# Kernel tuning notes

Hardware: AMD Instinct MI355X
Metric: run time of the kernel (lower is better)

## Reference

```python
import jax, jax.numpy as jnp
import numpy as np

EPS = 1e-5

def dwconv(x, w):
    # x: (B,C,T), w: (C,1,3) depthwise, stride 1, pad 1
    return jax.lax.conv_general_dilated(
        x, w, window_strides=(1,), padding=[(1, 1)],
        dimension_numbers=('NCH', 'OIH', 'NCH'),
        feature_group_count=x.shape[1])

def chan_ln(x, w, b):
    # LayerNorm over channel dim (axis=1) of (B,C,T)
    mu = jnp.mean(x, axis=1, keepdims=True)
    r = x - mu
    sigma = jnp.mean(r * r, axis=1, keepdims=True)
    return (r / jnp.sqrt(sigma + EPS)) * w + b

def conv1x1(x, w, b):
    # x: (B,C,T), w: (O,C), b: (O,)
    return jnp.einsum('oc,bct->bot', w, x) + b[None, :, None]

def setup_inputs() -> dict:
    B, C, T, H = 4, 1024, 1024, 16
    key0 = jax.random.key(0)
    ks = jax.random.split(key0, 16)
    s = 0.02
    inp = {
        'query': jax.random.normal(ks[0], (B, C, T), jnp.float32),
        'key': jax.random.normal(ks[1], (B, C, T), jnp.float32),
        'value': jax.random.normal(ks[2], (B, C, T), jnp.float32),
        'query_mask': jnp.ones((B, 1, T), jnp.bool_),
        'kv_mask': jnp.ones((B, 1, T), jnp.bool_),
        # depthwise conv weights (C,1,3), no bias
        'qconv_w': jax.random.normal(ks[3], (C, 1, 3), jnp.float32) * s,
        'kconv_w': jax.random.normal(ks[4], (C, 1, 3), jnp.float32) * s,
        'vconv_w': jax.random.normal(ks[5], (C, 1, 3), jnp.float32) * s,
        # channel LayerNorm affine params (1,C,1)
        'qn_w': jnp.ones((1, C, 1), jnp.float32), 'qn_b': jnp.zeros((1, C, 1), jnp.float32),
        'kn_w': jnp.ones((1, C, 1), jnp.float32), 'kn_b': jnp.zeros((1, C, 1), jnp.float32),
        'vn_w': jnp.ones((1, C, 1), jnp.float32), 'vn_b': jnp.zeros((1, C, 1), jnp.float32),
        # 1x1 conv (= per-timestep linear) weights (C,C) + bias (C,)
        'wq': jax.random.normal(ks[6], (C, C), jnp.float32) * s, 'bq': jnp.zeros((C,), jnp.float32),
        'wk': jax.random.normal(ks[7], (C, C), jnp.float32) * s, 'bk': jnp.zeros((C,), jnp.float32),
        'wv': jax.random.normal(ks[8], (C, C), jnp.float32) * s, 'bv': jnp.zeros((C,), jnp.float32),
        'wp': jax.random.normal(ks[9], (C, C), jnp.float32) * s, 'bp': jnp.zeros((C,), jnp.float32),
    }
    return inp

def reference(query, key, value, query_mask, kv_mask,
              qconv_w, kconv_w, vconv_w,
              qn_w, qn_b, kn_w, kn_b, vn_w, vn_b,
              wq, bq, wk, bk, wv, bv, wp, bp):
    B, C, T = query.shape
    H = 16
    ch = C // H
    scale = 1.0 / jnp.sqrt(jnp.asarray(ch, query.dtype))
    qm = query_mask.astype(query.dtype)   # (B,1,T), stride 1 -> qx_mask == query_mask
    kvm = kv_mask.astype(query.dtype)

    q = chan_ln(dwconv(query, qconv_w) * qm, qn_w, qn_b)
    k = chan_ln(dwconv(key, kconv_w) * kvm, kn_w, kn_b)
    v = chan_ln(dwconv(value, vconv_w) * kvm, vn_w, vn_b)

    q = conv1x1(q, wq, bq)
    k = conv1x1(k, wk, bk)
    v = conv1x1(v, wv, bv)

    # (B,C,T) -> (B,H,T,ch)
    q = q.reshape(B, H, ch, T).transpose(0, 1, 3, 2)
    k = k.reshape(B, H, ch, T).transpose(0, 1, 3, 2)
    v = v.reshape(B, H, ch, T).transpose(0, 1, 3, 2)

    att = jax.nn.softmax(jnp.einsum('bhsc,bhtc->bhst', q, k) * scale, axis=-1)
    # post-softmax mask applied to V (not to scores) — faithful to the original
    vm = v * kvm[:, :, :, None]           # (B,1,T)->(B,1,T,1) broadcast over heads/ch
    out = jnp.einsum('bhst,bhtc->bhsc', att, vm)

    out = out.transpose(0, 1, 3, 2).reshape(B, C, T)
    out = conv1x1(out, wp, bp) * qm
    return out, query_mask
```

## Files before the change

kernel.cpp:

```cpp
#include <hip/hip_runtime.h>
#include <math.h>

#define B_ 4
#define C_ 1024
#define T_ 1024
#define H_ 16
#define CH_ 64
#define BCT (B_ * C_ * T_)

typedef __attribute__((ext_vector_type(8))) short s16x8;
typedef __attribute__((ext_vector_type(4))) float f32x4;
typedef __attribute__((ext_vector_type(2))) float f32x2;
typedef unsigned short u16;
typedef unsigned char u8;

#define MFMA16(a, b, c) __builtin_amdgcn_mfma_f32_16x16x32_bf16((a), (b), (c), 0, 0, 0)
#define MFMA8(a, b, c)  __builtin_amdgcn_mfma_f32_16x16x32_fp8_fp8((a), (b), (c), 0, 0, 0)

extern "C" __device__ float __ocml_native_exp2_f32(float);

__device__ __forceinline__ u16 f2bf(float f) {
    union { float f; unsigned u; } v; v.f = f;
    unsigned r = (v.u + 0x7fffu + ((v.u >> 16) & 1u)) >> 16;
    return (u16)r;
}
__device__ __forceinline__ float bf2f(u16 h) {
    union { unsigned u; float f; } v; v.u = (unsigned)h << 16; return v.f;
}

__device__ __forceinline__ unsigned pk4_fp8(float a, float b, float c, float d) {
    int v = 0;
    v = __builtin_amdgcn_cvt_pk_fp8_f32(a, b, v, false);
    v = __builtin_amdgcn_cvt_pk_fp8_f32(c, d, v, true);
    return (unsigned)v;
}

typedef __attribute__((address_space(3))) unsigned int lds_u32;
typedef __attribute__((address_space(1))) const unsigned int glb_u32;
__device__ __forceinline__ void glds16(const void* g, const void* l_wave_uniform) {
    __builtin_amdgcn_global_load_lds(
        (glb_u32*)(unsigned long long)g,
        (lds_u32*)(unsigned long long)l_wave_uniform, 16, 0, 0);
}

#define WAIT_BARRIER(N)                                   \
    asm volatile("s_waitcnt vmcnt(" #N ")" ::: "memory"); \
    __builtin_amdgcn_s_barrier();                         \
    __builtin_amdgcn_sched_barrier(0)

__global__ __launch_bounds__(512) void prep_kernel(
    const float* __restrict__ xq, const float* __restrict__ xk, const float* __restrict__ xv,
    const float* __restrict__ wq3, const float* __restrict__ wk3, const float* __restrict__ wv3,
    const int* __restrict__ qm, const int* __restrict__ kvm,
    const float* __restrict__ qnw, const float* __restrict__ qnb,
    const float* __restrict__ knw, const float* __restrict__ knb,
    const float* __restrict__ vnw, const float* __restrict__ vnb,
    u8* __restrict__ oq, u8* __restrict__ ok, u8* __restrict__ ov,
    const float* __restrict__ w0, const float* __restrict__ w1,
    const float* __restrict__ w2, const float* __restrict__ w3,
    u8* __restrict__ o0, u8* __restrict__ o1, u8* __restrict__ o2, u16* __restrict__ o3,
    float* __restrict__ tail_out, int ntail)
{
    __shared__ __align__(16) u8 tile8[32 * 1040];
    __shared__ float w3L[3072];
    __shared__ float red1[16][33], red2[16][33];
    __shared__ float musL[32], rssL[32];

    const int bid = blockIdx.x;
    if (bid >= 384) {
        if (bid >= 2432) {
            int i = (bid - 2432) * 512 + threadIdx.x;
            if (i < ntail) tail_out[i] = (qm[i] != 0) ? 1.f : 0.f;
            return;
        }
        const int b2 = bid - 384;
        const int mat = b2 >> 9;
        const int i = ((b2 & 511) * 512 + threadIdx.x) * 4;
        if (mat == 3) {
            float4 v = *(const float4*)&w3[i];
            uint2 p;
            p.x = (unsigned)f2bf(v.x) | ((unsigned)f2bf(v.y) << 16);
            p.y = (unsigned)f2bf(v.z) | ((unsigned)f2bf(v.w) << 16);
            *(uint2*)&o3[i] = p;
        } else {
            const float* __restrict__ w = (mat == 0) ? w0 : (mat == 1) ? w1 : w2;
            u8* __restrict__ o = (mat == 0) ? o0 : (mat == 1) ? o1 : o2;
            float4 v = *(const float4*)&w[i];
            *(unsigned*)&o[i] = pk4_fp8(64.f * v.x, 64.f * v.y, 64.f * v.z, 64.f * v.w);
        }
        return;
    }

    const int z = bid >> 5;
    const int tensor = z >> 2, b = z & 3;
    const float* __restrict__ x   = (tensor == 0) ? xq  : (tensor == 1) ? xk  : xv;
    const float* __restrict__ w3c = (tensor == 0) ? wq3 : (tensor == 1) ? wk3 : wv3;
    const int* __restrict__ msk   = (tensor == 0) ? qm  : kvm;
    const float* __restrict__ wln = (tensor == 0) ? qnw : (tensor == 1) ? knw : vnw;
    const float* __restrict__ bln = (tensor == 0) ? qnb : (tensor == 1) ? knb : vnb;
    u8* __restrict__ xt = (tensor == 0) ? oq : (tensor == 1) ? ok : ov;

    const int t0 = (bid & 31) * 32;

    #pragma unroll
    for (int i = 0; i < 6; ++i) w3L[i * 512 + threadIdx.x] = w3c[i * 512 + threadIdx.x];
    __syncthreads();

    const int tl = threadIdx.x & 31, cs = threadIdx.x >> 5;
    const int t = t0 + tl;
    const float mk = (msk[b * T_ + t] != 0) ? 1.f : 0.f;

    float s1 = 0.f, s2 = 0.f;
    #pragma unroll 4
    for (int i = 0; i < 32; ++i) {
        const int c = 2 * (cs + 16 * i);
        const float* xr0 = x + ((size_t)(b * C_ + c)) * T_ + t;
        const float* xr1 = xr0 + T_;
        const f32x2 wA = *(const f32x2*)&w3L[3 * c];
        const f32x2 wB = *(const f32x2*)&w3L[3 * c + 2];
        const f32x2 wC = *(const f32x2*)&w3L[3 * c + 4];
        float xc0 = xr0[0];
        float xm0 = (t > 0)      ? xr0[-1] : 0.f;
        float xp0 = (t < T_ - 1) ? xr0[1]  : 0.f;
        float v0 = (wA[0] * xm0 + wA[1] * xc0 + wB[0] * xp0) * mk;
        float xc1 = xr1[0];
        float xm1 = (t > 0)      ? xr1[-1] : 0.f;
        float xp1 = (t < T_ - 1) ? xr1[1]  : 0.f;
        float v1 = (wB[1] * xm1 + wC[0] * xc1 + wC[1] * xp1) * mk;
        s1 += v0 + v1;
        s2 += v0 * v0 + v1 * v1;
        int p2 = __builtin_amdgcn_cvt_pk_fp8_f32(16.f * v0, 16.f * v1, 0, false);
        *(u16*)&tile8[tl * 1040 + c] = (u16)p2;
    }
    red1[cs][tl] = s1;
    red2[cs][tl] = s2;
    __syncthreads();
    if (threadIdx.x < 32) {
        float a = 0.f, q2 = 0.f;
        #pragma unroll
        for (int i = 0; i < 16; ++i) { a += red1[i][threadIdx.x]; q2 += red2[i][threadIdx.x]; }
        float m_  = a  * (1.f / C_);
        float var = q2 * (1.f / C_) - m_ * m_;
        musL[threadIdx.x] = m_;
        rssL[threadIdx.x] = rsqrtf(var + 1e-5f);
    }
    __syncthreads();

    #pragma unroll
    for (int it = 0; it < 8; ++it) {
        const int idx = it * 512 + threadIdx.x;
        const int tt = idx >> 7, c0 = (idx & 127) * 8;
        const uint2 pv8 = *(const uint2*)&tile8[tt * 1040 + c0];
        const f32x2 f01 = __builtin_amdgcn_cvt_pk_f32_fp8((int)pv8.x, false);
        const f32x2 f23 = __builtin_amdgcn_cvt_pk_f32_fp8((int)pv8.x, true);
        const f32x2 f45 = __builtin_amdgcn_cvt_pk_f32_fp8((int)pv8.y, false);
        const f32x2 f67 = __builtin_amdgcn_cvt_pk_f32_fp8((int)pv8.y, true);
        const float m_ = musL[tt], rv = rssL[tt];
        const float4 wv0 = *(const float4*)&wln[c0];
        const float4 wv1 = *(const float4*)&wln[c0 + 4];
        const float4 bv0 = *(const float4*)&bln[c0];
        const float4 bv1 = *(const float4*)&bln[c0 + 4];
        const float inv16 = 0.0625f;
        float fv0 = (f01[0] * inv16 - m_) * rv * wv0.x + bv0.x;
        float fv1 = (f01[1] * inv16 - m_) * rv * wv0.y + bv0.y;
        float fv2 = (f23[0] * inv16 - m_) * rv * wv0.z + bv0.z;
        float fv3 = (f23[1] * inv16 - m_) * rv * wv0.w + bv0.w;
        float fv4 = (f45[0] * inv16 - m_) * rv * wv1.x + bv1.x;
        float fv5 = (f45[1] * inv16 - m_) * rv * wv1.y + bv1.y;
        float fv6 = (f67[0] * inv16 - m_) * rv * wv1.z + bv1.z;
        float fv7 = (f67[1] * inv16 - m_) * rv * wv1.w + bv1.w;
        uint2 o;
        o.x = pk4_fp8(fv0, fv1, fv2, fv3);
        o.y = pk4_fp8(fv4, fv5, fv6, fv7);
        *(uint2*)&xt[((size_t)(b * T_ + t0 + tt)) * C_ + c0] = o;
    }
}

__device__ __forceinline__ void stage_slab8(
    const u8* __restrict__ gA, const u8* __restrict__ gB,
    u8* lA, u8* lB, int k0, int wave, int lane)
{
    const int rl = lane >> 1, h = lane & 1;
    const int row = wave * 32 + rl;
    const int hs = (h ^ ((row >> 2) & 1)) * 16;
    glds16(gA + (size_t)row * C_ + k0 + hs, lA + wave * 1024);
    glds16(gB + (size_t)row * C_ + k0 + hs, lB + wave * 1024);
}

__global__ __launch_bounds__(256) void gemm_qkv_kernel(
    const u8* __restrict__ Xq, const u8* __restrict__ Xk, const u8* __restrict__ Xv,
    const u8* __restrict__ Wq, const u8* __restrict__ Wk, const u8* __restrict__ Wv,
    const float* __restrict__ bq, const float* __restrict__ bk, const float* __restrict__ bv,
    u16* __restrict__ Qt, u16* __restrict__ Kt, u16* __restrict__ Vb, const int* __restrict__ kvm)
{
    const int p = blockIdx.x;
    const int lb = (p & 7) * 96 + (p >> 3);
    const int z = lb >> 6, yy = (lb >> 3) & 7, xx = lb & 7;
    const int tensor = z >> 2, b = z & 3;
    const size_t off = (size_t)b * (1024 * 1024);
    const float qscale = 0.125f * 1.44269504088896340736f;
    const u8* A = (tensor == 0) ? Xq + off : (tensor == 1) ? Xk + off : Wv;
    const u8* B = (tensor == 0) ? Wq       : (tensor == 1) ? Wk       : Xv + off;
    u16*     D = (tensor == 0) ? Qt + off : (tensor == 1) ? Kt + off : Vb + off;
    const float* bias = (tensor == 0) ? bq : (tensor == 1) ? bk : bv;
    const int* mask = (tensor == 2) ? kvm + (size_t)b * T_ : nullptr;
    const float scale = (tensor == 0) ? qscale : 1.f;
    const int bias_on_n = (tensor != 2);
    const int m0 = yy * 128, n0 = xx * 128;

    __shared__ __align__(16) u8 As[3][128 * 32];
    __shared__ __align__(16) u8 Bs[3][128 * 32];
    const int tid = threadIdx.x, lane = tid & 63, wave = tid >> 6;
    const int r = lane & 15, g = lane >> 4;
    const int wm = (wave >> 1) * 64, wn = (wave & 1) * 64;
    const u8* Ab = A + (size_t)m0 * C_;
    const u8* Bb = B + (size_t)n0 * C_;

    f32x4 acc[4][4];
    #pragma unroll
    for (int i = 0; i < 4; ++i)
        #pragma unroll
        for (int j = 0; j < 4; ++j) acc[i][j] = f32x4{0.f, 0.f, 0.f, 0.f};

    stage_slab8(Ab, Bb, As[0], Bs[0], 0, wave, lane);
    stage_slab8(Ab, Bb, As[1], Bs[1], 32, wave, lane);
    WAIT_BARRIER(2);

    const int rsw = ((r >> 2) & 1) << 1;
    const int NK = C_ / 32;
    int cur = 0;
    for (int kk = 0; kk < NK; ++kk) {
        int pre = cur + 2; if (pre >= 3) pre -= 3;
        if (kk + 2 < NK)
            stage_slab8(Ab, Bb, As[pre], Bs[pre], (kk + 2) * 32, wave, lane);
        long af[4], bf[4];
        #pragma unroll
        for (int mi = 0; mi < 4; ++mi)
            af[mi] = *(const long*)&As[cur][(wm + 16 * mi + r) * 32 + ((g ^ rsw) * 8)];
        #pragma unroll
        for (int ni = 0; ni < 4; ++ni)
            bf[ni] = *(const long*)&Bs[cur][(wn + 16 * ni + r) * 32 + ((g ^ rsw) * 8)];
        #pragma unroll
        for (int mi = 0; mi < 4; ++mi)
            #pragma unroll
            for (int ni = 0; ni < 4; ++ni)
                acc[mi][ni] = MFMA8(af[mi], bf[ni], acc[mi][ni]);
        if (kk + 1 < NK) {
            if (kk + 2 < NK) { WAIT_BARRIER(2); }
            else             { WAIT_BARRIER(0); }
        }
        cur = (cur == 2) ? 0 : cur + 1;
    }

    #pragma unroll
    for (int mi = 0; mi < 4; ++mi) {
        #pragma unroll
        for (int ni = 0; ni < 4; ++ni) {
            const int n = n0 + wn + 16 * ni + r;
            float mk = 1.f;
            if (mask) mk = (mask[n] != 0) ? 1.f : 0.f;
            #pragma unroll
            for (int i = 0; i < 4; ++i) {
                const int m = m0 + wm + 16 * mi + 4 * g + i;
                float v = acc[mi][ni][i] * 0.015625f + (bias_on_n ? bias[n] : bias[m]);
                v *= scale * mk;
                D[(size_t)m * 1024 + n] = f2bf(v);
            }
        }
    }
}

__device__ __forceinline__ void stage_slab(
    const u16* __restrict__ gA, const u16* __restrict__ gB,
    u16* lA, u16* lB, int k0, int wave, int lane)
{
    const int rw = lane >> 2, ch = lane & 3;
    const int sw = ((ch ^ ((rw >> 1) & 3)) * 8) + k0;
    const int r0 = 16 * wave + rw, r1 = r0 + 64;
    glds16(gA + (size_t)r0 * C_ + sw, lA + (16 * wave) * 32);
    glds16(gA + (size_t)r1 * C_ + sw, lA + (64 + 16 * wave) * 32);
    glds16(gB + (size_t)r0 * C_ + sw, lB + (16 * wave) * 32);
    glds16(gB + (size_t)r1 * C_ + sw, lB + (64 + 16 * wave) * 32);
}

__global__ __launch_bounds__(256) void gemm_out_kernel(
    const u16* __restrict__ Wp, const u16* __restrict__ att,
    const float* __restrict__ bp, float* __restrict__ out, const int* __restrict__ qm)
{
    const int p = blockIdx.x;
    const int lb = (p & 7) * 32 + (p >> 3);
    const int b = lb >> 6, yy = (lb >> 3) & 7, xx = lb & 7;
    const size_t off = (size_t)b * (1024 * 1024);
    const int m0 = yy * 128, n0 = xx * 128;
    const u16* Ab = Wp + (size_t)m0 * C_;
    const u16* Bb = att + off + (size_t)n0 * C_;
    float* D = out + off;
    const int* mask = qm + (size_t)b * T_;

    __shared__ __align__(16) u16 As[3][128 * 32];
    __shared__ __align__(16) u16 Bs[3][128 * 32];
    const int tid = threadIdx.x, lane = tid & 63, wave = tid >> 6;
    const int r = lane & 15, g = lane >> 4;
    const int wm = (wave >> 1) * 64, wn = (wave & 1) * 64;

    f32x4 acc[4][4];
    #pragma unroll
    for (int i = 0; i < 4; ++i)
        #pragma unroll
        for (int j = 0; j < 4; ++j) acc[i][j] = f32x4{0.f, 0.f, 0.f, 0.f};

    stage_slab(Ab, Bb, As[0], Bs[0], 0, wave, lane);
    stage_slab(Ab, Bb, As[1], Bs[1], 32, wave, lane);
    WAIT_BARRIER(4);

    const int swz = (g ^ ((r >> 1) & 3)) * 8;
    const int NK = C_ / 32;
    int cur = 0;
    for (int kk = 0; kk < NK; ++kk) {
        int pre = cur + 2; if (pre >= 3) pre -= 3;
        if (kk + 2 < NK)
            stage_slab(Ab, Bb, As[pre], Bs[pre], (kk + 2) * 32, wave, lane);
        s16x8 af[4], bf[4];
        #pragma unroll
        for (int mi = 0; mi < 4; ++mi)
            af[mi] = *(const s16x8*)&As[cur][(wm + 16 * mi + r) * 32 + swz];
        #pragma unroll
        for (int ni = 0; ni < 4; ++ni)
            bf[ni] = *(const s16x8*)&Bs[cur][(wn + 16 * ni + r) * 32 + swz];
        #pragma unroll
        for (int mi = 0; mi < 4; ++mi)
            #pragma unroll
            for (int ni = 0; ni < 4; ++ni)
                acc[mi][ni] = MFMA16(af[mi], bf[ni], acc[mi][ni]);
        if (kk + 1 < NK) {
            if (kk + 2 < NK) { WAIT_BARRIER(4); }
            else             { WAIT_BARRIER(0); }
        }
        cur = (cur == 2) ? 0 : cur + 1;
    }

    #pragma unroll
    for (int mi = 0; mi < 4; ++mi) {
        #pragma unroll
        for (int ni = 0; ni < 4; ++ni) {
            const int n = n0 + wn + 16 * ni + r;
            const float mk = (mask[n] != 0) ? 1.f : 0.f;
            #pragma unroll
            for (int i = 0; i < 4; ++i) {
                const int m = m0 + wm + 16 * mi + 4 * g + i;
                float v = (acc[mi][ni][i] + bp[m]) * mk;
                D[(size_t)m * 1024 + n] = v;
            }
        }
    }
}

__global__ __launch_bounds__(256) void attn_mfma_kernel(
    const u16* __restrict__ Qt, const u16* __restrict__ Kt, const u16* __restrict__ Vb,
    u16* __restrict__ att)
{
    const int p = blockIdx.x;
    const int lb = (p & 7) * 64 + (p >> 3);
    const int bh = lb >> 3, sblk = lb & 7;
    const int b = bh >> 4, h = bh & 15;
    const int lane = threadIdx.x & 63, wave = threadIdx.x >> 6;
    const int r = lane & 15, g = lane >> 4;
    const int hofs = h * 64;
    const int s0 = sblk * 128 + wave * 16;

    __shared__ __align__(16) u16 Ks[3][64 * 64];
    __shared__ __align__(16) u16 Vs[3][64 * 64];
    __shared__ __align__(16) u16 P_lds[4][2][16 * 72];

    const u16* qb0 = Qt + ((size_t)(b * T_ + s0 + r)) * C_ + hofs + g * 8;
    const s16x8 qf00 = *(const s16x8*)(qb0);
    const s16x8 qf01 = *(const s16x8*)(qb0 + 32);
    const s16x8 qf10 = *(const s16x8*)(qb0 + (size_t)64 * C_);
    const s16x8 qf11 = *(const s16x8*)(qb0 + (size_t)64 * C_ + 32);

    const int srow = lane >> 3, sch = lane & 7;
    const u16* kg = Kt + ((size_t)(b * T_)) * C_ + hofs;
    const u16* vg = Vb + ((size_t)(b * C_ + hofs)) * T_;

    auto stage = [&](int buf, int t0) {
        #pragma unroll
        for (int i = 0; i < 2; ++i) {
            const int rr = 16 * wave + 8 * i + srow;
            const int sw = (sch ^ (rr & 7)) * 8;
            glds16(kg + (size_t)(t0 + rr) * C_ + sw, &Ks[buf][(16 * wave + 8 * i) * 64]);
            glds16(vg + (size_t)rr * T_ + t0 + sw,   &Vs[buf][(16 * wave + 8 * i) * 64]);
        }
    };

    f32x4 acc0[4], acc1[4];
    #pragma unroll
    for (int ci = 0; ci < 4; ++ci) {
        acc0[ci] = f32x4{0.f, 0.f, 0.f, 0.f};
        acc1[ci] = f32x4{0.f, 0.f, 0.f, 0.f};
    }
    float l0 = 0.f, l1 = 0.f;
    u16* pw0 = &P_lds[wave][0][0];
    u16* pw1 = &P_lds[wave][1][0];

    stage(0, 0);
    stage(1, 64);
    WAIT_BARRIER(4);

    const int NT = T_ / 64;
    int cur = 0;
    for (int it = 0; it < NT; ++it) {
        int pre = cur + 2; if (pre >= 3) pre -= 3;
        if (it + 2 < NT) stage(pre, (it + 2) * 64);

        const u16* ks = Ks[cur];
        f32x4 st0[4], st1[4];
        __builtin_amdgcn_s_setprio(1);
        #pragma unroll
        for (int tt = 0; tt < 4; ++tt) {
            const int row = (16 * tt + r) * 64;
            const s16x8 ka = *(const s16x8*)&ks[row + ((g ^ (r & 7)) * 8)];
            const s16x8 kb = *(const s16x8*)&ks[row + (((4 + g) ^ (r & 7)) * 8)];
            f32x4 sa = f32x4{0.f, 0.f, 0.f, 0.f};
            sa = MFMA16(ka, qf00, sa); sa = MFMA16(kb, qf01, sa); st0[tt] = sa;
            f32x4 sb = f32x4{0.f, 0.f, 0.f, 0.f};
            sb = MFMA16(ka, qf10, sb); sb = MFMA16(kb, qf11, sb); st1[tt] = sb;
        }
        __builtin_amdgcn_s_setprio(0);

        #pragma unroll
        for (int tt = 0; tt < 4; ++tt) {
            float a0 = __ocml_native_exp2_f32(st0[tt][0]);
            float a1 = __ocml_native_exp2_f32(st0[tt][1]);
            float a2 = __ocml_native_exp2_f32(st0[tt][2]);
            float a3 = __ocml_native_exp2_f32(st0[tt][3]);
            l0 += (a0 + a1) + (a2 + a3);
            uint2 pk;
            pk.x = (unsigned)f2bf(a0) | ((unsigned)f2bf(a1) << 16);
            pk.y = (unsigned)f2bf(a2) | ((unsigned)f2bf(a3) << 16);
            *(uint2*)&pw0[r * 72 + 16 * tt + 4 * g] = pk;
            float b0 = __ocml_native_exp2_f32(st1[tt][0]);
            float b1 = __ocml_native_exp2_f32(st1[tt][1]);
            float b2 = __ocml_native_exp2_f32(st1[tt][2]);
            float b3 = __ocml_native_exp2_f32(st1[tt][3]);
            l1 += (b0 + b1) + (b2 + b3);
            pk.x = (unsigned)f2bf(b0) | ((unsigned)f2bf(b1) << 16);
            pk.y = (unsigned)f2bf(b2) | ((unsigned)f2bf(b3) << 16);
            *(uint2*)&pw1[r * 72 + 16 * tt + 4 * g] = pk;
        }

        const u16* vs = Vs[cur];
        __builtin_amdgcn_s_setprio(1);
        #pragma unroll
        for (int kk = 0; kk < 2; ++kk) {
            const s16x8 pa0 = *(const s16x8*)&pw0[r * 72 + 32 * kk + 8 * g];
            const s16x8 pa1 = *(const s16x8*)&pw1[r * 72 + 32 * kk + 8 * g];
            #pragma unroll
            for (int ci = 0; ci < 4; ++ci) {
                const s16x8 vf = *(const s16x8*)
                    &vs[(16 * ci + r) * 64 + (((4 * kk + g) ^ (r & 7)) * 8)];
                acc0[ci] = MFMA16(pa0, vf, acc0[ci]);
                acc1[ci] = MFMA16(pa1, vf, acc1[ci]);
            }
        }
        __builtin_amdgcn_s_setprio(0);

        if (it + 1 < NT) {
            if (it + 2 < NT) { WAIT_BARRIER(4); }
            else             { WAIT_BARRIER(0); }
        }
        cur = (cur == 2) ? 0 : cur + 1;
    }

    l0 += __shfl_xor(l0, 16); l0 += __shfl_xor(l0, 32);
    l1 += __shfl_xor(l1, 16); l1 += __shfl_xor(l1, 32);
    const float inv0 = 1.f / l0, inv1 = 1.f / l1;
    const float i00 = __shfl(inv0, 4 * g + 0), i01 = __shfl(inv0, 4 * g + 1);
    const float i02 = __shfl(inv0, 4 * g + 2), i03 = __shfl(inv0, 4 * g + 3);
    const float i10 = __shfl(inv1, 4 * g + 0), i11 = __shfl(inv1, 4 * g + 1);
    const float i12 = __shfl(inv1, 4 * g + 2), i13 = __shfl(inv1, 4 * g + 3);

    u16* ob = att + ((size_t)(b * T_ + s0 + 4 * g)) * C_ + hofs + r;
    #pragma unroll
    for (int ci = 0; ci < 4; ++ci) {
        ob[(size_t)0 * C_ + ci * 16] = f2bf(acc0[ci][0] * i00);
        ob[(size_t)1 * C_ + ci * 16] = f2bf(acc0[ci][1] * i01);
        ob[(size_t)2 * C_ + ci * 16] = f2bf(acc0[ci][2] * i02);
        ob[(size_t)3 * C_ + ci * 16] = f2bf(acc0[ci][3] * i03);
    }
    u16* ob1 = ob + (size_t)64 * C_;
    #pragma unroll
    for (int ci = 0; ci < 4; ++ci) {
        ob1[(size_t)0 * C_ + ci * 16] = f2bf(acc1[ci][0] * i10);
        ob1[(size_t)1 * C_ + ci * 16] = f2bf(acc1[ci][1] * i11);
        ob1[(size_t)2 * C_ + ci * 16] = f2bf(acc1[ci][2] * i12);
        ob1[(size_t)3 * C_ + ci * 16] = f2bf(acc1[ci][3] * i13);
    }
}

extern "C" void kernel_launch(void* const* d_in, const int* in_sizes, int n_in,
                              void* d_out, int out_size, void* d_ws, size_t ws_size,
                              hipStream_t stream)
{
    const float* query = (const float*)d_in[0];
    const float* key_  = (const float*)d_in[1];
    const float* value = (const float*)d_in[2];
    const int* qm  = (const int*)d_in[3];
    const int* kvm = (const int*)d_in[4];
    const float* qconv = (const float*)d_in[5];
    const float* kconv = (const float*)d_in[6];
    const float* vconv = (const float*)d_in[7];
    const float* qnw = (const float*)d_in[8];
    const float* qnb = (const float*)d_in[9];
    const float* knw = (const float*)d_in[10];
    const float* knb = (const float*)d_in[11];
    const float* vnw = (const float*)d_in[12];
    const float* vnb = (const float*)d_in[13];
    const float* wq = (const float*)d_in[14];
    const float* bq = (const float*)d_in[15];
    const float* wk = (const float*)d_in[16];
    const float* bk = (const float*)d_in[17];
    const float* wv = (const float*)d_in[18];
    const float* bv = (const float*)d_in[19];
    const float* wp = (const float*)d_in[20];
    const float* bp = (const float*)d_in[21];

    const size_t MB = 1024 * 1024;
    char* W = (char*)d_ws;
    u8* Xq   = (u8*)(W + 0 * MB);
    u8* Xk   = (u8*)(W + 8 * MB);
    u8* Xv   = (u8*)(W + 16 * MB);
    u16* Qt  = (u16*)(W + 24 * MB);
    u16* Kt  = (u16*)(W + 32 * MB);
    u16* Vb_ = (u16*)(W + 40 * MB);
    u16* att_ = (u16*)(W + 48 * MB);
    u8* wq8  = (u8*)(W + 56 * MB);
    u8* wk8  = (u8*)(W + 58 * MB);
    u8* wv8  = (u8*)(W + 60 * MB);
    u16* wpb = (u16*)(W + 62 * MB);

    int ntail = out_size - BCT;
    if (ntail < 0) ntail = 0;

    prep_kernel<<<dim3(2440), 512, 0, stream>>>(
        query, key_, value, qconv, kconv, vconv, qm, kvm,
        qnw, qnb, knw, knb, vnw, vnb, Xq, Xk, Xv,
        wq, wk, wv, wp, wq8, wk8, wv8, wpb,
        (float*)d_out + BCT, ntail);

    gemm_qkv_kernel<<<dim3(768), 256, 0, stream>>>(
        Xq, Xk, Xv, wq8, wk8, wv8, bq, bk, bv, Qt, Kt, Vb_, kvm);

    attn_mfma_kernel<<<dim3(512), 256, 0, stream>>>(Qt, Kt, Vb_, att_);

    gemm_out_kernel<<<dim3(256), 256, 0, stream>>>(wpb, att_, bp, (float*)d_out, qm);
}
```

Before: 115.6 us.

## Store Q/K/V as FP8 and run attention MFMAs in FP8

The QKV GEMM epilogue now writes Q, K and V as FP8 instead of bf16. Q and K are each scaled by the square root of the combined softmax/log2 factor. The attention kernel stages FP8 K/V tiles with a new swizzle, keeps P in FP8 in LDS, and uses fp8 16x16x32 MFMAs for both QK^T and PV. This halves attention memory traffic and LDS footprint, at the cost of accuracy from FP8 quantization of Q, K, V and the softmax probabilities.

```diff
diff --git a/kernel.cpp b/kernel.cpp
--- a/kernel.cpp
+++ b/kernel.cpp
@@ -191,20 +191,20 @@
     const u8* __restrict__ Xq, const u8* __restrict__ Xk, const u8* __restrict__ Xv,
     const u8* __restrict__ Wq, const u8* __restrict__ Wk, const u8* __restrict__ Wv,
     const float* __restrict__ bq, const float* __restrict__ bk, const float* __restrict__ bv,
-    u16* __restrict__ Qt, u16* __restrict__ Kt, u16* __restrict__ Vb, const int* __restrict__ kvm)
+    u8* __restrict__ Qt, u8* __restrict__ Kt, u8* __restrict__ Vb, const int* __restrict__ kvm)
 {
     const int p = blockIdx.x;
     const int lb = (p & 7) * 96 + (p >> 3);
     const int z = lb >> 6, yy = (lb >> 3) & 7, xx = lb & 7;
     const int tensor = z >> 2, b = z & 3;
     const size_t off = (size_t)b * (1024 * 1024);
-    const float qscale = 0.125f * 1.44269504088896340736f;
+    const float qkscale = 0.42466090f;
     const u8* A = (tensor == 0) ? Xq + off : (tensor == 1) ? Xk + off : Wv;
     const u8* B = (tensor == 0) ? Wq       : (tensor == 1) ? Wk       : Xv + off;
-    u16*     D = (tensor == 0) ? Qt + off : (tensor == 1) ? Kt + off : Vb + off;
+    u8*      D = (tensor == 0) ? Qt + off : (tensor == 1) ? Kt + off : Vb + off;
     const float* bias = (tensor == 0) ? bq : (tensor == 1) ? bk : bv;
     const int* mask = (tensor == 2) ? kvm + (size_t)b * T_ : nullptr;
-    const float scale = (tensor == 0) ? qscale : 1.f;
+    const float scale = (tensor == 2) ? 1.f : qkscale;
     const int bias_on_n = (tensor != 2);
     const int m0 = yy * 128, n0 = xx * 128;
 
@@ -264,7 +264,8 @@
                 const int m = m0 + wm + 16 * mi + 4 * g + i;
                 float v = acc[mi][ni][i] * 0.015625f + (bias_on_n ? bias[n] : bias[m]);
                 v *= scale * mk;
-                D[(size_t)m * 1024 + n] = f2bf(v);
+                int pk = __builtin_amdgcn_cvt_pk_fp8_f32(v, v, 0, false);
+                D[(size_t)m * 1024 + n] = (u8)(pk & 0xff);
             }
         }
     }
@@ -356,7 +357,7 @@
 }
 
 __global__ __launch_bounds__(256) void attn_mfma_kernel(
-    const u16* __restrict__ Qt, const u16* __restrict__ Kt, const u16* __restrict__ Vb,
+    const u8* __restrict__ Qt, const u8* __restrict__ Kt, const u8* __restrict__ Vb,
     u16* __restrict__ att)
 {
     const int p = blockIdx.x;
@@ -368,28 +369,24 @@
     const int hofs = h * 64;
     const int s0 = sblk * 128 + wave * 16;
 
-    __shared__ __align__(16) u16 Ks[3][64 * 64];
-    __shared__ __align__(16) u16 Vs[3][64 * 64];
-    __shared__ __align__(16) u16 P_lds[4][2][16 * 72];
-
-    const u16* qb0 = Qt + ((size_t)(b * T_ + s0 + r)) * C_ + hofs + g * 8;
-    const s16x8 qf00 = *(const s16x8*)(qb0);
-    const s16x8 qf01 = *(const s16x8*)(qb0 + 32);
-    const s16x8 qf10 = *(const s16x8*)(qb0 + (size_t)64 * C_);
-    const s16x8 qf11 = *(const s16x8*)(qb0 + (size_t)64 * C_ + 32);
-
-    const int srow = lane >> 3, sch = lane & 7;
-    const u16* kg = Kt + ((size_t)(b * T_)) * C_ + hofs;
-    const u16* vg = Vb + ((size_t)(b * C_ + hofs)) * T_;
+    __shared__ __align__(16) u8 Ks[3][64 * 64];
+    __shared__ __align__(16) u8 Vs[3][64 * 64];
+    __shared__ __align__(16) u8 P8[4][2][16 * 72];
+
+    const u8* qb0 = Qt + ((size_t)(b * T_ + s0 + r)) * C_ + hofs + g * 8;
+    const long qf00 = *(const long*)(qb0);
+    const long qf01 = *(const long*)(qb0 + 32);
+    const long qf10 = *(const long*)(qb0 + (size_t)64 * C_);
+    const long qf11 = *(const long*)(qb0 + (size_t)64 * C_ + 32);
+
+    const int rr = 16 * wave + (lane >> 2);
+    const int sb16 = ((lane & 3) ^ ((rr >> 1) & 3)) * 16;
+    const u8* kg = Kt + ((size_t)(b * T_)) * C_ + hofs;
+    const u8* vg = Vb + ((size_t)(b * C_ + hofs)) * T_;
 
     auto stage = [&](int buf, int t0) {
-        #pragma unroll
-        for (int i = 0; i < 2; ++i) {
-            const int rr = 16 * wave + 8 * i + srow;
-            const int sw = (sch ^ (rr & 7)) * 8;
-            glds16(kg + (size_t)(t0 + rr) * C_ + sw, &Ks[buf][(16 * wave + 8 * i) * 64]);
-            glds16(vg + (size_t)rr * T_ + t0 + sw,   &Vs[buf][(16 * wave + 8 * i) * 64]);
-        }
+        glds16(kg + (size_t)(t0 + rr) * C_ + sb16, &Ks[buf][(16 * wave) * 64]);
+        glds16(vg + (size_t)rr * T_ + t0 + sb16,   &Vs[buf][(16 * wave) * 64]);
     };
 
     f32x4 acc0[4], acc1[4];
@@ -399,12 +396,12 @@
         acc1[ci] = f32x4{0.f, 0.f, 0.f, 0.f};
     }
     float l0 = 0.f, l1 = 0.f;
-    u16* pw0 = &P_lds[wave][0][0];
-    u16* pw1 = &P_lds[wave][1][0];
+    u8* pw0 = &P8[wave][0][0];
+    u8* pw1 = &P8[wave][1][0];
 
     stage(0, 0);
     stage(1, 64);
-    WAIT_BARRIER(4);
+    WAIT_BARRIER(2);
 
     const int NT = T_ / 64;
     int cur = 0;
@@ -412,18 +409,21 @@
         int pre = cur + 2; if (pre >= 3) pre -= 3;
         if (it + 2 < NT) stage(pre, (it + 2) * 64);
 
-        const u16* ks = Ks[cur];
+        const u8* ks = Ks[cur];
         f32x4 st0[4], st1[4];
         __builtin_amdgcn_s_setprio(1);
         #pragma unroll
         for (int tt = 0; tt < 4; ++tt) {
-            const int row = (16 * tt + r) * 64;
-            const s16x8 ka = *(const s16x8*)&ks[row + ((g ^ (r & 7)) * 8)];
-            const s16x8 kb = *(const s16x8*)&ks[row + (((4 + g) ^ (r & 7)) * 8)];
+            const int rowk = 16 * tt + r;
+            const int ph = (rowk >> 1) & 3;
+            const long ka = *(const long*)
+                &ks[rowk * 64 + (((g >> 1) ^ ph) * 16 + (g & 1) * 8)];
+            const long kb = *(const long*)
+                &ks[rowk * 64 + (((2 + (g >> 1)) ^ ph) * 16 + (g & 1) * 8)];
             f32x4 sa = f32x4{0.f, 0.f, 0.f, 0.f};
-            sa = MFMA16(ka, qf00, sa); sa = MFMA16(kb, qf01, sa); st0[tt] = sa;
+            sa = MFMA8(ka, qf00, sa); sa = MFMA8(kb, qf01, sa); st0[tt] = sa;
             f32x4 sb = f32x4{0.f, 0.f, 0.f, 0.f};
-            sb = MFMA16(ka, qf10, sb); sb = MFMA16(kb, qf11, sb); st1[tt] = sb;
+            sb = MFMA8(ka, qf10, sb); sb = MFMA8(kb, qf11, sb); st1[tt] = sb;
         }
         __builtin_amdgcn_s_setprio(0);
 
@@ -434,38 +434,35 @@
             float a2 = __ocml_native_exp2_f32(st0[tt][2]);
             float a3 = __ocml_native_exp2_f32(st0[tt][3]);
             l0 += (a0 + a1) + (a2 + a3);
-            uint2 pk;
-            pk.x = (unsigned)f2bf(a0) | ((unsigned)f2bf(a1) << 16);
-            pk.y = (unsigned)f2bf(a2) | ((unsigned)f2bf(a3) << 16);
-            *(uint2*)&pw0[r * 72 + 16 * tt + 4 * g] = pk;
+            *(unsigned*)&pw0[r * 72 + 16 * tt + 4 * g] = pk4_fp8(a0, a1, a2, a3);
             float b0 = __ocml_native_exp2_f32(st1[tt][0]);
             float b1 = __ocml_native_exp2_f32(st1[tt][1]);
             float b2 = __ocml_native_exp2_f32(st1[tt][2]);
             float b3 = __ocml_native_exp2_f32(st1[tt][3]);
             l1 += (b0 + b1) + (b2 + b3);
-            pk.x = (unsigned)f2bf(b0) | ((unsigned)f2bf(b1) << 16);
-            pk.y = (unsigned)f2bf(b2) | ((unsigned)f2bf(b3) << 16);
-            *(uint2*)&pw1[r * 72 + 16 * tt + 4 * g] = pk;
-        }
-
-        const u16* vs = Vs[cur];
+            *(unsigned*)&pw1[r * 72 + 16 * tt + 4 * g] = pk4_fp8(b0, b1, b2, b3);
+        }
+
+        const u8* vs = Vs[cur];
         __builtin_amdgcn_s_setprio(1);
         #pragma unroll
         for (int kk = 0; kk < 2; ++kk) {
-            const s16x8 pa0 = *(const s16x8*)&pw0[r * 72 + 32 * kk + 8 * g];
-            const s16x8 pa1 = *(const s16x8*)&pw1[r * 72 + 32 * kk + 8 * g];
+            const long pa0 = *(const long*)&pw0[r * 72 + 32 * kk + 8 * g];
+            const long pa1 = *(const long*)&pw1[r * 72 + 32 * kk + 8 * g];
             #pragma unroll
             for (int ci = 0; ci < 4; ++ci) {
-                const s16x8 vf = *(const s16x8*)
-                    &vs[(16 * ci + r) * 64 + (((4 * kk + g) ^ (r & 7)) * 8)];
-                acc0[ci] = MFMA16(pa0, vf, acc0[ci]);
-                acc1[ci] = MFMA16(pa1, vf, acc1[ci]);
+                const int rowv = 16 * ci + r;
+                const int pv_ = (rowv >> 1) & 3;
+                const long vf = *(const long*)
+                    &vs[rowv * 64 + (((2 * kk + (g >> 1)) ^ pv_) * 16 + (g & 1) * 8)];
+                acc0[ci] = MFMA8(pa0, vf, acc0[ci]);
+                acc1[ci] = MFMA8(pa1, vf, acc1[ci]);
             }
         }
         __builtin_amdgcn_s_setprio(0);
 
         if (it + 1 < NT) {
-            if (it + 2 < NT) { WAIT_BARRIER(4); }
+            if (it + 2 < NT) { WAIT_BARRIER(2); }
             else             { WAIT_BARRIER(0); }
         }
         cur = (cur == 2) ? 0 : cur + 1;
@@ -529,9 +526,9 @@
     u8* Xq   = (u8*)(W + 0 * MB);
     u8* Xk   = (u8*)(W + 8 * MB);
     u8* Xv   = (u8*)(W + 16 * MB);
-    u16* Qt  = (u16*)(W + 24 * MB);
-    u16* Kt  = (u16*)(W + 32 * MB);
-    u16* Vb_ = (u16*)(W + 40 * MB);
+    u8* Qt   = (u8*)(W + 24 * MB);
+    u8* Kt   = (u8*)(W + 32 * MB);
+    u8* Vb_  = (u8*)(W + 40 * MB);
     u16* att_ = (u16*)(W + 48 * MB);
     u8* wq8  = (u8*)(W + 56 * MB);
     u8* wk8  = (u8*)(W + 58 * MB);
```

After: 107.8 us. -6.8%, faster.
